# Kernel tuning notes

Hardware: AMD Instinct MI355X
Metric: run time of the kernel (lower is better)

The kernel has to match this reference:

```python
import jax, jax.numpy as jnp
import numpy as np

INF = 10000.0
HEAD_SIZE = 64
HEADS = 12


def _rope_tables(seqlen, dim, dtype=jnp.float32):
    inv_freq = 1.0 / (10000.0 ** (jnp.arange(0, dim, 2, dtype=dtype) / dim))
    t = jnp.arange(seqlen, dtype=dtype)
    freqs = t[:, None] * inv_freq[None, :]  # [n, dim//2]
    return jnp.sin(freqs), jnp.cos(freqs)


def _apply_rope(t, sin, cos):
    # t: [b, n, d]; sin/cos: [n, d//2]
    t1, t2 = t[..., 0::2], t[..., 1::2]
    r1 = t1 * cos - t2 * sin
    r2 = t1 * sin + t2 * cos
    return jnp.stack([r1, r2], axis=-1).reshape(t.shape)


def setup_inputs() -> dict:
    key = jax.random.key(0)
    k1, k2, k3, k4, k5, k6 = jax.random.split(key, 6)
    B, N, H = 16, 512, 1024
    inputs = jax.random.normal(k1, (B, N, H), dtype=jnp.float32)
    attention_mask = jax.random.randint(k2, (B, N), 0, 2, dtype=jnp.int32)
    w1 = jax.random.normal(k3, (H, 2 * HEAD_SIZE), dtype=jnp.float32) * 0.02
    b1 = jax.random.normal(k4, (2 * HEAD_SIZE,), dtype=jnp.float32) * 0.02
    w2 = jax.random.normal(k5, (2 * HEAD_SIZE, 2 * HEADS), dtype=jnp.float32) * 0.02
    b2 = jax.random.normal(k6, (2 * HEADS,), dtype=jnp.float32) * 0.02
    return {"inputs": inputs, "attention_mask": attention_mask,
            "w1": w1, "b1": b1, "w2": w2, "b2": b2}


def reference(inputs, attention_mask, w1, b1, w2, b2):
    B, N, _ = inputs.shape
    x = inputs @ w1 + b1  # [b, n, 2*head_size]
    qw, kw = x[..., 0::2], x[..., 1::2]  # each [b, n, head_size]
    sin, cos = _rope_tables(N, HEAD_SIZE, x.dtype)
    qw = _apply_rope(qw, sin, cos)
    kw = _apply_rope(kw, sin, cos)
    logits = jnp.einsum('bmd,bnd->bmn', qw, kw) / (HEAD_SIZE ** 0.5)
    bias = jnp.swapaxes(x @ w2 + b2, 1, 2) / 2.0  # [b, 2*heads, n]
    logits = logits[:, None] + bias[:, 0::2, None, :] + bias[:, 1::2, :, None]  # [b, h, m, n]
    am = attention_mask.astype(logits.dtype)
    pad_mask = 1.0 - am[:, None, None, :] * am[:, None, :, None]
    logits = logits - pad_mask * INF
    idx = jnp.arange(N)
    tril = (idx[:, None] > idx[None, :]).astype(logits.dtype)  # strict lower triangle
    logits = logits - tril * INF
    return logits
```

## Files before the change

### kernel.cpp

```cpp
#include <hip/hip_runtime.h>

typedef __bf16 bf16_t;
typedef bf16_t bf16x4 __attribute__((ext_vector_type(4)));
typedef bf16_t bf16x8 __attribute__((ext_vector_type(8)));
typedef float f32x4 __attribute__((ext_vector_type(4)));

#define INFV 10000.0f

__global__ __launch_bounds__(256) void k0_transpose(const float* __restrict__ w1,
                                                    bf16_t* __restrict__ w1T) {
    __shared__ float s[32][36];
    const int t = threadIdx.x;
    const int k0 = (blockIdx.x & 31) * 32;
    const int c0 = (blockIdx.x >> 5) * 32;
    {
        const int r = t >> 3, cc = (t & 7) * 4;
        *(float4*)&s[r][cc] = *(const float4*)&w1[(size_t)(k0 + r) * 128 + c0 + cc];
    }
    __syncthreads();
    {
        const int cr = t >> 3, kk = (t & 7) * 4;
        bf16x4 v;
        v[0] = (bf16_t)s[kk + 0][cr];
        v[1] = (bf16_t)s[kk + 1][cr];
        v[2] = (bf16_t)s[kk + 2][cr];
        v[3] = (bf16_t)s[kk + 3][cr];
        *(bf16x4*)&w1T[(size_t)(c0 + cr) * 1024 + k0 + kk] = v;
    }
}

__global__ __launch_bounds__(256) void k1_proj(
    const float* __restrict__ inputs,
    const bf16_t* __restrict__ w1T,
    const float* __restrict__ b1,
    const float* __restrict__ w2,
    const float* __restrict__ b2,
    bf16_t* __restrict__ qg,
    bf16_t* __restrict__ kg,
    float* __restrict__ biasT)
{
    __shared__ bf16_t s_a[16][72];
    __shared__ float s_x[16][132];
    __shared__ float s_w2T[24][132];

    const int t = threadIdx.x;
    const int row0 = blockIdx.x * 16;
    const int lane = t & 63, wave = t >> 6;
    const int cn = lane & 15, kgrp = lane >> 4;

    for (int i = t; i < 3072; i += 256) {
        int j = i / 24, c = i - j * 24;
        s_w2T[c][j] = w2[i];
    }

    f32x4 acc[2] = {};
    const int sr = t >> 4;
    const int sc = (t & 15) * 4;
    float4 pf = *(const float4*)&inputs[(size_t)(row0 + sr) * 1024 + sc];

    for (int ks = 0; ks < 16; ++ks) {
        const int k0 = ks * 64;
        {
            bf16x4 v;
            v[0] = (bf16_t)pf.x; v[1] = (bf16_t)pf.y; v[2] = (bf16_t)pf.z; v[3] = (bf16_t)pf.w;
            *(bf16x4*)&s_a[sr][sc] = v;
        }
        __syncthreads();
        if (ks < 15)
            pf = *(const float4*)&inputs[(size_t)(row0 + sr) * 1024 + k0 + 64 + sc];
        bf16x8 a0 = *(const bf16x8*)&s_a[cn][kgrp * 8];
        bf16x8 a1 = *(const bf16x8*)&s_a[cn][32 + kgrp * 8];
#pragma unroll
        for (int tt = 0; tt < 2; ++tt) {
            const int col = wave * 32 + tt * 16 + cn;
            const bf16_t* wp = w1T + (size_t)col * 1024 + k0 + kgrp * 8;
            bf16x8 bb0 = *(const bf16x8*)wp;
            bf16x8 bb1 = *(const bf16x8*)(wp + 32);
            acc[tt] = __builtin_amdgcn_mfma_f32_16x16x32_bf16(a0, bb0, acc[tt], 0, 0, 0);
            acc[tt] = __builtin_amdgcn_mfma_f32_16x16x32_bf16(a1, bb1, acc[tt], 0, 0, 0);
        }
        __syncthreads();
    }

    {
        const int rgrp = lane >> 4;
#pragma unroll
        for (int tt = 0; tt < 2; ++tt) {
            const int col = wave * 32 + tt * 16 + cn;
            const float bb = b1[col];
#pragma unroll
            for (int r = 0; r < 4; ++r)
                s_x[rgrp * 4 + r][col] = acc[tt][r] + bb;
        }
    }
    __syncthreads();

    {
        const int r = t >> 4;
        const int i0 = (t & 15) * 2;
        const int rowg = row0 + r;
        const int n = rowg & 511;
        bf16x4 qv, kv;
#pragma unroll
        for (int u = 0; u < 2; ++u) {
            const int i = i0 + u;
            float fr = (float)n * exp2f((float)i * -0.4152410118609203f);
            float sv, cv;
            sincosf(fr, &sv, &cv);
            float x0 = s_x[r][4 * i + 0];
            float x1 = s_x[r][4 * i + 1];
            float x2 = s_x[r][4 * i + 2];
            float x3 = s_x[r][4 * i + 3];
            qv[2 * u]     = (bf16_t)(x0 * cv - x2 * sv);
            qv[2 * u + 1] = (bf16_t)(x0 * sv + x2 * cv);
            kv[2 * u]     = (bf16_t)(x1 * cv - x3 * sv);
            kv[2 * u + 1] = (bf16_t)(x1 * sv + x3 * cv);
        }
        *(bf16x4*)&qg[(size_t)rowg * 64 + 2 * i0] = qv;
        *(bf16x4*)&kg[(size_t)rowg * 64 + 2 * i0] = kv;
    }

    {
        const int r = t >> 4;
        const int cb = t & 15;
        if (cb < 12) {
            const int c0 = cb * 2;
            float sum0 = 0.f, sum1 = 0.f;
#pragma unroll 4
            for (int j = 0; j < 128; j += 4) {
                float4 xv = *(const float4*)&s_x[r][j];
                float4 wa = *(const float4*)&s_w2T[c0 + 0][j];
                float4 wb = *(const float4*)&s_w2T[c0 + 1][j];
                sum0 += xv.x * wa.x + xv.y * wa.y + xv.z * wa.z + xv.w * wa.w;
                sum1 += xv.x * wb.x + xv.y * wb.y + xv.z * wb.z + xv.w * wb.w;
            }
            const int rowg = row0 + r;
            const int bb = rowg >> 9, n = rowg & 511;
            float* bp = biasT + (size_t)bb * 12288 + n;
            bp[(size_t)(c0 + 0) * 512] = (sum0 + b2[c0 + 0]) * 0.5f;
            bp[(size_t)(c0 + 1) * 512] = (sum1 + b2[c0 + 1]) * 0.5f;
        }
    }
}

__global__ __launch_bounds__(256) void k2_logits(
    const bf16_t* __restrict__ qg, const bf16_t* __restrict__ kg,
    const float* __restrict__ biasT, const int* __restrict__ am,
    float* __restrict__ out)
{
    __shared__ float s_be[12][64], s_bo[12][64];
    __shared__ float s_pm[64], s_pn[64];

    const int t = threadIdx.x;
    const int b = blockIdx.z;
    const int m0 = blockIdx.y * 64;
    const int n0 = blockIdx.x * 64;

    for (int i = t; i < 768; i += 256) {
        const int h = i >> 6, j = i & 63;
        s_be[h][j] = biasT[(size_t)b * 12288 + (size_t)(2 * h) * 512 + n0 + j];
        s_bo[h][j] = biasT[(size_t)b * 12288 + (size_t)(2 * h + 1) * 512 + m0 + j];
    }
    if (t < 64) s_pm[t] = (float)am[b * 512 + m0 + t];
    else if (t < 128) s_pn[t - 64] = (float)am[b * 512 + n0 + (t - 64)];

    const int lane = t & 63, wave = t >> 6;
    const int cn = lane & 15, kgrp = lane >> 4;

    const bf16_t* qp = qg + ((size_t)(b * 512 + m0 + wave * 16 + cn)) * 64 + kgrp * 8;
    bf16x8 qb0 = *(const bf16x8*)qp;
    bf16x8 qb1 = *(const bf16x8*)(qp + 32);

    f32x4 acc[4] = {};
#pragma unroll
    for (int nt = 0; nt < 4; ++nt) {
        const bf16_t* kp = kg + ((size_t)(b * 512 + n0 + nt * 16 + cn)) * 64 + kgrp * 8;
        bf16x8 ka0 = *(const bf16x8*)kp;
        bf16x8 ka1 = *(const bf16x8*)(kp + 32);
        acc[nt] = __builtin_amdgcn_mfma_f32_16x16x32_bf16(ka0, qb0, acc[nt], 0, 0, 0);
        acc[nt] = __builtin_amdgcn_mfma_f32_16x16x32_bf16(ka1, qb1, acc[nt], 0, 0, 0);
    }
    __syncthreads();

    const int rgrp = lane >> 4;
    const int m_loc = wave * 16 + cn;
    const int m = m0 + m_loc;
    const float am_m = s_pm[m_loc];

#pragma unroll
    for (int nt = 0; nt < 4; ++nt) {
#pragma unroll
        for (int r = 0; r < 4; ++r) {
            const int n_loc = nt * 16 + rgrp * 4 + r;
            float v = acc[nt][r] * 0.125f;
            v -= (1.0f - am_m * s_pn[n_loc]) * INFV;
            if (m > n0 + n_loc) v -= INFV;
            acc[nt][r] = v;
        }
    }

    float* ob = out + (size_t)b * 3145728 + (size_t)m * 512 + n0;
#pragma unroll
    for (int h = 0; h < 12; ++h) {
        const float bo = s_bo[h][m_loc];
        const f32x4 bov = {bo, bo, bo, bo};
#pragma unroll
        for (int nt = 0; nt < 4; ++nt) {
            const f32x4 be4 = *(const f32x4*)&s_be[h][nt * 16 + rgrp * 4];
            f32x4 w = acc[nt] + be4 + bov;
            *(f32x4*)&ob[(size_t)h * 262144 + nt * 16 + rgrp * 4] = w;
        }
    }
}

extern "C" void kernel_launch(void* const* d_in, const int* in_sizes, int n_in,
                              void* d_out, int out_size, void* d_ws, size_t ws_size,
                              hipStream_t stream) {
    const float* inputs = (const float*)d_in[0];
    const int*   am     = (const int*)d_in[1];
    const float* w1     = (const float*)d_in[2];
    const float* b1     = (const float*)d_in[3];
    const float* w2     = (const float*)d_in[4];
    const float* b2     = (const float*)d_in[5];
    float* out = (float*)d_out;

    bf16_t* w1T   = (bf16_t*)d_ws;
    bf16_t* qg    = w1T + 131072;
    bf16_t* kg    = qg + 524288;
    float*  biasT = (float*)(kg + 524288);

    k0_transpose<<<128, 256, 0, stream>>>(w1, w1T);
    k1_proj<<<512, 256, 0, stream>>>(inputs, w1T, b1, w2, b2, qg, kg, biasT);
    k2_logits<<<dim3(8, 8, 16), 256, 0, stream>>>(qg, kg, biasT, am, out);
}
```

Before: 67.71 us.

## Stream projection operands straight into registers and fuse RoPE into the MFMA epilogue

The projection kernel no longer stages input rows through shared memory with two barriers per k-step. Each lane now loads its fp32 input fragment and bf16 weight fragment directly from global memory, software-prefetched one step ahead, and feeds them to MFMA with the weight as the A operand so the accumulator comes out row-major per lane. RoPE is applied right from the accumulator registers using fast __sinf/__cosf, which removes the separate shared-memory pass and the precise sincos. The trade-off is reduced accuracy of the fast sin/cos at large angles, and input loads that may coalesce worse.

```diff
diff --git a/kernel.cpp b/kernel.cpp
--- a/kernel.cpp
+++ b/kernel.cpp
@@ -1,6 +1,7 @@
 #include <hip/hip_runtime.h>
 
 typedef __bf16 bf16_t;
+typedef bf16_t bf16x2 __attribute__((ext_vector_type(2)));
 typedef bf16_t bf16x4 __attribute__((ext_vector_type(4)));
 typedef bf16_t bf16x8 __attribute__((ext_vector_type(8)));
 typedef float f32x4 __attribute__((ext_vector_type(4)));
@@ -39,7 +40,6 @@
     bf16_t* __restrict__ kg,
     float* __restrict__ biasT)
 {
-    __shared__ bf16_t s_a[16][72];
     __shared__ float s_x[16][132];
     __shared__ float s_w2T[24][132];
 
@@ -53,72 +53,57 @@
         s_w2T[c][j] = w2[i];
     }
 
+    const int m = row0 + cn;
+    const float* ap = inputs + (size_t)m * 1024 + kgrp * 8;
+    const int colbase = wave * 32;
+    const bf16_t* bp0 = w1T + (size_t)(colbase + cn) * 1024 + kgrp * 8;
+    const bf16_t* bp1 = bp0 + 16 * 1024;
+
     f32x4 acc[2] = {};
-    const int sr = t >> 4;
-    const int sc = (t & 15) * 4;
-    float4 pf = *(const float4*)&inputs[(size_t)(row0 + sr) * 1024 + sc];
-
-    for (int ks = 0; ks < 16; ++ks) {
-        const int k0 = ks * 64;
-        {
-            bf16x4 v;
-            v[0] = (bf16_t)pf.x; v[1] = (bf16_t)pf.y; v[2] = (bf16_t)pf.z; v[3] = (bf16_t)pf.w;
-            *(bf16x4*)&s_a[sr][sc] = v;
-        }
-        __syncthreads();
-        if (ks < 15)
-            pf = *(const float4*)&inputs[(size_t)(row0 + sr) * 1024 + k0 + 64 + sc];
-        bf16x8 a0 = *(const bf16x8*)&s_a[cn][kgrp * 8];
-        bf16x8 a1 = *(const bf16x8*)&s_a[cn][32 + kgrp * 8];
-#pragma unroll
-        for (int tt = 0; tt < 2; ++tt) {
-            const int col = wave * 32 + tt * 16 + cn;
-            const bf16_t* wp = w1T + (size_t)col * 1024 + k0 + kgrp * 8;
-            bf16x8 bb0 = *(const bf16x8*)wp;
-            bf16x8 bb1 = *(const bf16x8*)(wp + 32);
-            acc[tt] = __builtin_amdgcn_mfma_f32_16x16x32_bf16(a0, bb0, acc[tt], 0, 0, 0);
-            acc[tt] = __builtin_amdgcn_mfma_f32_16x16x32_bf16(a1, bb1, acc[tt], 0, 0, 0);
-        }
-        __syncthreads();
-    }
-
-    {
-        const int rgrp = lane >> 4;
-#pragma unroll
-        for (int tt = 0; tt < 2; ++tt) {
-            const int col = wave * 32 + tt * 16 + cn;
-            const float bb = b1[col];
-#pragma unroll
-            for (int r = 0; r < 4; ++r)
-                s_x[rgrp * 4 + r][col] = acc[tt][r] + bb;
-        }
+
+    float4 pa0 = *(const float4*)(ap);
+    float4 pa1 = *(const float4*)(ap + 4);
+    bf16x8 pb0 = *(const bf16x8*)(bp0);
+    bf16x8 pb1 = *(const bf16x8*)(bp1);
+
+#pragma unroll 4
+    for (int ks = 0; ks < 32; ++ks) {
+        float4 ca0 = pa0, ca1 = pa1;
+        bf16x8 cb0 = pb0, cb1 = pb1;
+        if (ks < 31) {
+            const int o = (ks + 1) * 32;
+            pa0 = *(const float4*)(ap + o);
+            pa1 = *(const float4*)(ap + o + 4);
+            pb0 = *(const bf16x8*)(bp0 + o);
+            pb1 = *(const bf16x8*)(bp1 + o);
+        }
+        bf16x8 af;
+        af[0] = (bf16_t)ca0.x; af[1] = (bf16_t)ca0.y; af[2] = (bf16_t)ca0.z; af[3] = (bf16_t)ca0.w;
+        af[4] = (bf16_t)ca1.x; af[5] = (bf16_t)ca1.y; af[6] = (bf16_t)ca1.z; af[7] = (bf16_t)ca1.w;
+        acc[0] = __builtin_amdgcn_mfma_f32_16x16x32_bf16(cb0, af, acc[0], 0, 0, 0);
+        acc[1] = __builtin_amdgcn_mfma_f32_16x16x32_bf16(cb1, af, acc[1], 0, 0, 0);
+    }
+
+    const int rgrp = kgrp;
+    const int nseq = m & 511;
+#pragma unroll
+    for (int tt = 0; tt < 2; ++tt) {
+        const int c0 = colbase + tt * 16 + rgrp * 4;
+        f32x4 bv = *(const f32x4*)&b1[c0];
+        f32x4 x = acc[tt] + bv;
+        *(f32x4*)&s_x[cn][c0] = x;
+        const int i = c0 >> 2;
+        float fr = (float)nseq * exp2f((float)i * -0.4152410118609203f);
+        float sv = __sinf(fr), cv = __cosf(fr);
+        bf16x2 qv, kv;
+        qv[0] = (bf16_t)(x[0] * cv - x[2] * sv);
+        qv[1] = (bf16_t)(x[0] * sv + x[2] * cv);
+        kv[0] = (bf16_t)(x[1] * cv - x[3] * sv);
+        kv[1] = (bf16_t)(x[1] * sv + x[3] * cv);
+        *(bf16x2*)&qg[(size_t)m * 64 + 2 * i] = qv;
+        *(bf16x2*)&kg[(size_t)m * 64 + 2 * i] = kv;
     }
     __syncthreads();
-
-    {
-        const int r = t >> 4;
-        const int i0 = (t & 15) * 2;
-        const int rowg = row0 + r;
-        const int n = rowg & 511;
-        bf16x4 qv, kv;
-#pragma unroll
-        for (int u = 0; u < 2; ++u) {
-            const int i = i0 + u;
-            float fr = (float)n * exp2f((float)i * -0.4152410118609203f);
-            float sv, cv;
-            sincosf(fr, &sv, &cv);
-            float x0 = s_x[r][4 * i + 0];
-            float x1 = s_x[r][4 * i + 1];
-            float x2 = s_x[r][4 * i + 2];
-            float x3 = s_x[r][4 * i + 3];
-            qv[2 * u]     = (bf16_t)(x0 * cv - x2 * sv);
-            qv[2 * u + 1] = (bf16_t)(x0 * sv + x2 * cv);
-            kv[2 * u]     = (bf16_t)(x1 * cv - x3 * sv);
-            kv[2 * u + 1] = (bf16_t)(x1 * sv + x3 * cv);
-        }
-        *(bf16x4*)&qg[(size_t)rowg * 64 + 2 * i0] = qv;
-        *(bf16x4*)&kg[(size_t)rowg * 64 + 2 * i0] = kv;
-    }
 
     {
         const int r = t >> 4;
```

After: 80.65 us. 19.1% more time.

## Stage full input row tile in swizzled LDS and use fast sin/cos

Applied to the files above, without the earlier changes.

The projection kernel now loads all 16x1024 input rows into LDS as bf16 at once, using an XOR swizzle against bank conflicts. The MFMA loop then runs over 32 k-chunks with no per-step barriers, replacing the double-sync software pipeline. This enlarges shared memory to about 32KB for the A tile, which may lower occupancy, and front-loads all global reads. sincosf is also replaced with the lower-precision __sinf/__cosf intrinsics, which trades RoPE accuracy at large arguments for speed.

```diff
diff --git a/kernel.cpp b/kernel.cpp
--- a/kernel.cpp
+++ b/kernel.cpp
@@ -1,6 +1,7 @@
 #include <hip/hip_runtime.h>
 
 typedef __bf16 bf16_t;
+typedef bf16_t bf16x2 __attribute__((ext_vector_type(2)));
 typedef bf16_t bf16x4 __attribute__((ext_vector_type(4)));
 typedef bf16_t bf16x8 __attribute__((ext_vector_type(8)));
 typedef float f32x4 __attribute__((ext_vector_type(4)));
@@ -39,7 +40,7 @@
     bf16_t* __restrict__ kg,
     float* __restrict__ biasT)
 {
-    __shared__ bf16_t s_a[16][72];
+    __shared__ bf16_t s_a[16 * 1024];
     __shared__ float s_x[16][132];
     __shared__ float s_w2T[24][132];
 
@@ -53,40 +54,43 @@
         s_w2T[c][j] = w2[i];
     }
 
+    {
+        const int r = t >> 4, u = t & 15;
+        const float* src = inputs + (size_t)(row0 + r) * 1024;
+        char* drow = (char*)s_a + r * 2048;
+        const int sw = (r & 7) << 4;
+#pragma unroll
+        for (int j = 0; j < 16; ++j) {
+            const int col = j * 64 + u * 4;
+            float4 v = *(const float4*)&src[col];
+            bf16x4 b;
+            b[0] = (bf16_t)v.x; b[1] = (bf16_t)v.y; b[2] = (bf16_t)v.z; b[3] = (bf16_t)v.w;
+            *(bf16x4*)(drow + ((col * 2) ^ sw)) = b;
+        }
+    }
+    __syncthreads();
+
     f32x4 acc[2] = {};
-    const int sr = t >> 4;
-    const int sc = (t & 15) * 4;
-    float4 pf = *(const float4*)&inputs[(size_t)(row0 + sr) * 1024 + sc];
-
-    for (int ks = 0; ks < 16; ++ks) {
-        const int k0 = ks * 64;
-        {
-            bf16x4 v;
-            v[0] = (bf16_t)pf.x; v[1] = (bf16_t)pf.y; v[2] = (bf16_t)pf.z; v[3] = (bf16_t)pf.w;
-            *(bf16x4*)&s_a[sr][sc] = v;
-        }
-        __syncthreads();
-        if (ks < 15)
-            pf = *(const float4*)&inputs[(size_t)(row0 + sr) * 1024 + k0 + 64 + sc];
-        bf16x8 a0 = *(const bf16x8*)&s_a[cn][kgrp * 8];
-        bf16x8 a1 = *(const bf16x8*)&s_a[cn][32 + kgrp * 8];
+    const char* arow = (const char*)s_a + cn * 2048;
+    const int sw = (cn & 7) << 4;
+    const int colbase = wave * 32;
+    const bf16_t* bp0 = w1T + (size_t)(colbase + cn) * 1024 + kgrp * 8;
+    const bf16_t* bp1 = bp0 + 16 * 1024;
+
+#pragma unroll 8
+    for (int kc = 0; kc < 32; ++kc) {
+        bf16x8 af = *(const bf16x8*)(arow + ((kc * 64 + kgrp * 16) ^ sw));
+        bf16x8 b0 = *(const bf16x8*)(bp0 + kc * 32);
+        bf16x8 b1 = *(const bf16x8*)(bp1 + kc * 32);
+        acc[0] = __builtin_amdgcn_mfma_f32_16x16x32_bf16(af, b0, acc[0], 0, 0, 0);
+        acc[1] = __builtin_amdgcn_mfma_f32_16x16x32_bf16(af, b1, acc[1], 0, 0, 0);
+    }
+
+    {
+        const int rgrp = lane >> 4;
 #pragma unroll
         for (int tt = 0; tt < 2; ++tt) {
-            const int col = wave * 32 + tt * 16 + cn;
-            const bf16_t* wp = w1T + (size_t)col * 1024 + k0 + kgrp * 8;
-            bf16x8 bb0 = *(const bf16x8*)wp;
-            bf16x8 bb1 = *(const bf16x8*)(wp + 32);
-            acc[tt] = __builtin_amdgcn_mfma_f32_16x16x32_bf16(a0, bb0, acc[tt], 0, 0, 0);
-            acc[tt] = __builtin_amdgcn_mfma_f32_16x16x32_bf16(a1, bb1, acc[tt], 0, 0, 0);
-        }
-        __syncthreads();
-    }
-
-    {
-        const int rgrp = lane >> 4;
-#pragma unroll
-        for (int tt = 0; tt < 2; ++tt) {
-            const int col = wave * 32 + tt * 16 + cn;
+            const int col = colbase + tt * 16 + cn;
             const float bb = b1[col];
 #pragma unroll
             for (int r = 0; r < 4; ++r)
@@ -105,8 +109,7 @@
         for (int u = 0; u < 2; ++u) {
             const int i = i0 + u;
             float fr = (float)n * exp2f((float)i * -0.4152410118609203f);
-            float sv, cv;
-            sincosf(fr, &sv, &cv);
+            float sv = __sinf(fr), cv = __cosf(fr);
             float x0 = s_x[r][4 * i + 0];
             float x1 = s_x[r][4 * i + 1];
             float x2 = s_x[r][4 * i + 2];
```

After: 71.12 us. 5.0% more time.

## Restructure projection kernel to 512 threads with deeper prefetch and swizzled LDS

Applied to the files above, without the earlier changes.

The projection kernel now runs 8 waves per block, each owning one 16-column MFMA tile, and steps through K in 128-wide chunks with four float4 prefetch registers in flight. The A tile in LDS uses an XOR swizzle to avoid bank conflicts. The RoPE and bias epilogues are redistributed so each thread handles one frequency or one bias channel. The aim is more memory-level parallelism and fewer barriers on the input-read-bound GEMM, at the cost of more registers per thread and a larger block.

```diff
diff --git a/kernel.cpp b/kernel.cpp
--- a/kernel.cpp
+++ b/kernel.cpp
@@ -1,6 +1,7 @@
 #include <hip/hip_runtime.h>
 
 typedef __bf16 bf16_t;
+typedef bf16_t bf16x2 __attribute__((ext_vector_type(2)));
 typedef bf16_t bf16x4 __attribute__((ext_vector_type(4)));
 typedef bf16_t bf16x8 __attribute__((ext_vector_type(8)));
 typedef float f32x4 __attribute__((ext_vector_type(4)));
@@ -29,7 +30,7 @@
     }
 }
 
-__global__ __launch_bounds__(256) void k1_proj(
+__global__ __launch_bounds__(512) void k1_proj(
     const float* __restrict__ inputs,
     const bf16_t* __restrict__ w1T,
     const float* __restrict__ b1,
@@ -39,7 +40,7 @@
     bf16_t* __restrict__ kg,
     float* __restrict__ biasT)
 {
-    __shared__ bf16_t s_a[16][72];
+    __shared__ bf16_t s_a[16 * 128];
     __shared__ float s_x[16][132];
     __shared__ float s_w2T[24][132];
 
@@ -48,97 +49,105 @@
     const int lane = t & 63, wave = t >> 6;
     const int cn = lane & 15, kgrp = lane >> 4;
 
-    for (int i = t; i < 3072; i += 256) {
+    for (int i = t; i < 3072; i += 512) {
         int j = i / 24, c = i - j * 24;
         s_w2T[c][j] = w2[i];
     }
 
-    f32x4 acc[2] = {};
-    const int sr = t >> 4;
-    const int sc = (t & 15) * 4;
-    float4 pf = *(const float4*)&inputs[(size_t)(row0 + sr) * 1024 + sc];
-
-    for (int ks = 0; ks < 16; ++ks) {
-        const int k0 = ks * 64;
+    const int sr = t >> 5;
+    const int scb = (t & 31) * 8;
+    const float* bsrc = inputs + (size_t)(row0 + sr) * 1024 + (t & 31) * 4;
+    char* const sa = (char*)s_a;
+    const int wbyte = (sr * 256 + scb) ^ ((sr & 7) << 4);
+
+    f32x4 acc = {};
+    const bf16_t* bp = w1T + (size_t)(wave * 16 + cn) * 1024 + kgrp * 8;
+    const int rbyte0 = (cn * 256 + kgrp * 16) ^ ((cn & 7) << 4);
+
+    float4 pf0 = *(const float4*)(bsrc + 0 * 128);
+    float4 pf1 = *(const float4*)(bsrc + 1 * 128);
+    float4 pf2 = *(const float4*)(bsrc + 2 * 128);
+    float4 pf3 = *(const float4*)(bsrc + 3 * 128);
+
+#pragma unroll
+    for (int kt = 0; kt < 8; ++kt) {
+        float4 cur;
+        switch (kt & 3) {
+            case 0: cur = pf0; break;
+            case 1: cur = pf1; break;
+            case 2: cur = pf2; break;
+            default: cur = pf3; break;
+        }
         {
             bf16x4 v;
-            v[0] = (bf16_t)pf.x; v[1] = (bf16_t)pf.y; v[2] = (bf16_t)pf.z; v[3] = (bf16_t)pf.w;
-            *(bf16x4*)&s_a[sr][sc] = v;
+            v[0] = (bf16_t)cur.x; v[1] = (bf16_t)cur.y;
+            v[2] = (bf16_t)cur.z; v[3] = (bf16_t)cur.w;
+            *(bf16x4*)(sa + wbyte) = v;
         }
         __syncthreads();
-        if (ks < 15)
-            pf = *(const float4*)&inputs[(size_t)(row0 + sr) * 1024 + k0 + 64 + sc];
-        bf16x8 a0 = *(const bf16x8*)&s_a[cn][kgrp * 8];
-        bf16x8 a1 = *(const bf16x8*)&s_a[cn][32 + kgrp * 8];
-#pragma unroll
-        for (int tt = 0; tt < 2; ++tt) {
-            const int col = wave * 32 + tt * 16 + cn;
-            const bf16_t* wp = w1T + (size_t)col * 1024 + k0 + kgrp * 8;
-            bf16x8 bb0 = *(const bf16x8*)wp;
-            bf16x8 bb1 = *(const bf16x8*)(wp + 32);
-            acc[tt] = __builtin_amdgcn_mfma_f32_16x16x32_bf16(a0, bb0, acc[tt], 0, 0, 0);
-            acc[tt] = __builtin_amdgcn_mfma_f32_16x16x32_bf16(a1, bb1, acc[tt], 0, 0, 0);
+        if (kt < 4) {
+            const float4 nv = *(const float4*)(bsrc + (kt + 4) * 128);
+            switch (kt & 3) {
+                case 0: pf0 = nv; break;
+                case 1: pf1 = nv; break;
+                case 2: pf2 = nv; break;
+                default: pf3 = nv; break;
+            }
+        }
+        const int k0 = kt * 128;
+#pragma unroll
+        for (int kk = 0; kk < 4; ++kk) {
+            bf16x8 af = *(const bf16x8*)(sa + (rbyte0 ^ (kk * 64)));
+            bf16x8 bf = *(const bf16x8*)(bp + k0 + kk * 32);
+            acc = __builtin_amdgcn_mfma_f32_16x16x32_bf16(af, bf, acc, 0, 0, 0);
         }
         __syncthreads();
     }
 
     {
-        const int rgrp = lane >> 4;
-#pragma unroll
-        for (int tt = 0; tt < 2; ++tt) {
-            const int col = wave * 32 + tt * 16 + cn;
-            const float bb = b1[col];
-#pragma unroll
-            for (int r = 0; r < 4; ++r)
-                s_x[rgrp * 4 + r][col] = acc[tt][r] + bb;
-        }
+        const int col = wave * 16 + cn;
+        const float bb = b1[col];
+#pragma unroll
+        for (int r = 0; r < 4; ++r)
+            s_x[kgrp * 4 + r][col] = acc[r] + bb;
     }
     __syncthreads();
 
     {
-        const int r = t >> 4;
-        const int i0 = (t & 15) * 2;
+        const int r = t >> 5;
+        const int i = t & 31;
         const int rowg = row0 + r;
         const int n = rowg & 511;
-        bf16x4 qv, kv;
-#pragma unroll
-        for (int u = 0; u < 2; ++u) {
-            const int i = i0 + u;
-            float fr = (float)n * exp2f((float)i * -0.4152410118609203f);
-            float sv, cv;
-            sincosf(fr, &sv, &cv);
-            float x0 = s_x[r][4 * i + 0];
-            float x1 = s_x[r][4 * i + 1];
-            float x2 = s_x[r][4 * i + 2];
-            float x3 = s_x[r][4 * i + 3];
-            qv[2 * u]     = (bf16_t)(x0 * cv - x2 * sv);
-            qv[2 * u + 1] = (bf16_t)(x0 * sv + x2 * cv);
-            kv[2 * u]     = (bf16_t)(x1 * cv - x3 * sv);
-            kv[2 * u + 1] = (bf16_t)(x1 * sv + x3 * cv);
-        }
-        *(bf16x4*)&qg[(size_t)rowg * 64 + 2 * i0] = qv;
-        *(bf16x4*)&kg[(size_t)rowg * 64 + 2 * i0] = kv;
-    }
-
-    {
-        const int r = t >> 4;
-        const int cb = t & 15;
-        if (cb < 12) {
-            const int c0 = cb * 2;
-            float sum0 = 0.f, sum1 = 0.f;
+        float fr = (float)n * exp2f((float)i * -0.4152410118609203f);
+        float sv, cv;
+        sincosf(fr, &sv, &cv);
+        float x0 = s_x[r][4 * i + 0];
+        float x1 = s_x[r][4 * i + 1];
+        float x2 = s_x[r][4 * i + 2];
+        float x3 = s_x[r][4 * i + 3];
+        bf16x2 qv, kv;
+        qv[0] = (bf16_t)(x0 * cv - x2 * sv);
+        qv[1] = (bf16_t)(x0 * sv + x2 * cv);
+        kv[0] = (bf16_t)(x1 * cv - x3 * sv);
+        kv[1] = (bf16_t)(x1 * sv + x3 * cv);
+        *(bf16x2*)&qg[(size_t)rowg * 64 + 2 * i] = qv;
+        *(bf16x2*)&kg[(size_t)rowg * 64 + 2 * i] = kv;
+    }
+
+    {
+        const int r = t >> 5;
+        const int cb = t & 31;
+        if (cb < 24) {
+            float sum = 0.f;
 #pragma unroll 4
             for (int j = 0; j < 128; j += 4) {
                 float4 xv = *(const float4*)&s_x[r][j];
-                float4 wa = *(const float4*)&s_w2T[c0 + 0][j];
-                float4 wb = *(const float4*)&s_w2T[c0 + 1][j];
-                sum0 += xv.x * wa.x + xv.y * wa.y + xv.z * wa.z + xv.w * wa.w;
-                sum1 += xv.x * wb.x + xv.y * wb.y + xv.z * wb.z + xv.w * wb.w;
+                float4 wa = *(const float4*)&s_w2T[cb][j];
+                sum += xv.x * wa.x + xv.y * wa.y + xv.z * wa.z + xv.w * wa.w;
             }
             const int rowg = row0 + r;
             const int bb = rowg >> 9, n = rowg & 511;
-            float* bp = biasT + (size_t)bb * 12288 + n;
-            bp[(size_t)(c0 + 0) * 512] = (sum0 + b2[c0 + 0]) * 0.5f;
-            bp[(size_t)(c0 + 1) * 512] = (sum1 + b2[c0 + 1]) * 0.5f;
+            biasT[(size_t)bb * 12288 + (size_t)cb * 512 + n] = (sum + b2[cb]) * 0.5f;
         }
     }
 }
@@ -230,6 +239,6 @@
     float*  biasT = (float*)(kg + 524288);
 
     k0_transpose<<<128, 256, 0, stream>>>(w1, w1T);
-    k1_proj<<<512, 256, 0, stream>>>(inputs, w1T, b1, w2, b2, qg, kg, biasT);
+    k1_proj<<<512, 512, 0, stream>>>(inputs, w1T, b1, w2, b2, qg, kg, biasT);
     k2_logits<<<dim3(8, 8, 16), 256, 0, stream>>>(qg, kg, biasT, am, out);
 }
```

New measurement: 68.95 us. No clear change (+1.8%).
